# Kernel optimization log

Measured on AMD Instinct MI355X. Metric: run time of the kernel, lower is better.

Reference implementation:

```python
import jax, jax.numpy as jnp
import numpy as np

B, S, D, H, DK, DV = 2, 2048, 1024, 16, 64, 64


def setup_inputs() -> dict:
    key = jax.random.key(0)
    ks = jax.random.split(key, 12)
    s = 0.02
    return {
        "q": jax.random.normal(ks[0], (B, S, D), jnp.float32),
        "k": jax.random.normal(ks[1], (B, S, D), jnp.float32),
        "v": jax.random.normal(ks[2], (B, S, D), jnp.float32),
        "attn_mask": jax.random.bernoulli(ks[3], 0.1, (B, S, S)),
        "wq": jax.random.normal(ks[4], (D, H * DK), jnp.float32) * s,
        "bq": jnp.zeros((H * DK,), jnp.float32),
        "wk": jax.random.normal(ks[5], (D, H * DK), jnp.float32) * s,
        "bk": jnp.zeros((H * DK,), jnp.float32),
        "wv": jax.random.normal(ks[6], (D, H * DV), jnp.float32) * s,
        "bv": jnp.zeros((H * DV,), jnp.float32),
        "wo": jax.random.normal(ks[7], (H * DV, D), jnp.float32) * s,
        "bo": jnp.zeros((D,), jnp.float32),
        "gamma": jnp.ones((D,), jnp.float32),
        "beta": jnp.zeros((D,), jnp.float32),
    }


def reference(q, k, v, attn_mask, wq, bq, wk, bk, wv, bv, wo, bo, gamma, beta):
    residual = q
    # projections -> [B, H, S, dk/dv]
    qh = (q @ wq + bq).reshape(B, S, H, DK).transpose(0, 2, 1, 3)
    kh = (k @ wk + bk).reshape(B, S, H, DK).transpose(0, 2, 1, 3)
    vh = (v @ wv + bv).reshape(B, S, H, DV).transpose(0, 2, 1, 3)
    scores = jnp.einsum("bhqd,bhkd->bhqk", qh, kh) / np.sqrt(DK).astype(np.float32)
    scores = jnp.where(attn_mask[:, None, :, :], jnp.float32(-1e9), scores)
    attn = jax.nn.softmax(scores, axis=-1)
    context = jnp.einsum("bhqk,bhkd->bhqd", attn, vh)
    context = context.transpose(0, 2, 1, 3).reshape(B, S, H * DV)
    out = context @ wo + bo + residual
    # LayerNorm (eps=1e-5, torch default)
    mu = out.mean(-1, keepdims=True)
    var = out.var(-1, keepdims=True)
    out = (out - mu) * jax.lax.rsqrt(var + 1e-5) * gamma + beta
    return out, attn
```

## Files before the change

### kernel.cpp

```cpp
#include <hip/hip_runtime.h>
#include <hip/hip_bf16.h>

#define BB 2
#define SS 2048
#define DD 1024
#define HH 16
#define DKV 64

typedef __attribute__((ext_vector_type(8))) short short8;
typedef __attribute__((ext_vector_type(4))) short short4_t;
typedef __attribute__((ext_vector_type(4))) float f32x4;

#define MFMA16(a, b, c) __builtin_amdgcn_mfma_f32_16x16x32_bf16(a, b, c, 0, 0, 0)

__device__ __forceinline__ short f2bf(float f) {
    __hip_bfloat16 h = __float2bfloat16(f);
    union { __hip_bfloat16 h; short s; } u;
    u.h = h;
    return u.s;
}

__global__ __launch_bounds__(256) void proj3_kernel(
    const float* __restrict__ A0, const float* __restrict__ A1, const float* __restrict__ A2,
    const float* __restrict__ W0, const float* __restrict__ W1, const float* __restrict__ W2,
    const float* __restrict__ bq, const float* __restrict__ bk, const float* __restrict__ bv,
    __hip_bfloat16* __restrict__ o0, __hip_bfloat16* __restrict__ o1, __hip_bfloat16* __restrict__ o2,
    const int* __restrict__ mask, unsigned long long* __restrict__ bits)
{
    const int t = threadIdx.x;
    const int lane = t & 63;
    const int wave = t >> 6;

    if (blockIdx.z == 0) {
        const int bid = blockIdx.y * 32 + blockIdx.x;
        const int base = bid * 512 + wave * 128;
        #pragma unroll 4
        for (int wi = base; wi < base + 128; ++wi) {
            const int mv = mask[(size_t)wi * 64 + lane];
            const unsigned long long bal = __ballot(mv != 0);
            if (lane == 0) bits[wi] = bal;
        }
        return;
    }

    const int z = blockIdx.z - 1;
    const float* A = (z == 0) ? A0 : (z == 1) ? A1 : A2;
    const float* W = (z == 0) ? W0 : (z == 1) ? W1 : W2;
    const float* bias = (z == 0) ? bq : (z == 1) ? bk : bv;
    __hip_bfloat16* outh = (z == 0) ? o0 : (z == 1) ? o1 : o2;

    __shared__ __align__(16) short As[128][40];
    __shared__ __align__(16) short Bs[128][40];
    const int wm = wave >> 1, wn = wave & 1;
    const int m0 = blockIdx.x * 128, n0 = blockIdx.y * 128;
    const int lr = lane & 15;
    const int kb = (lane >> 4) * 8;

    f32x4 acc[4][4] = {};

    for (int k0 = 0; k0 < DD; k0 += 32) {
        __syncthreads();
        {
            const int row = t >> 1, kk = (t & 1) * 16;
            const float* src = A + (size_t)(m0 + row) * DD + k0 + kk;
            float4 fa = *(const float4*)(src);
            float4 fb = *(const float4*)(src + 4);
            float4 fc = *(const float4*)(src + 8);
            float4 fd = *(const float4*)(src + 12);
            short8 v0 = { f2bf(fa.x), f2bf(fa.y), f2bf(fa.z), f2bf(fa.w),
                          f2bf(fb.x), f2bf(fb.y), f2bf(fb.z), f2bf(fb.w) };
            short8 v1 = { f2bf(fc.x), f2bf(fc.y), f2bf(fc.z), f2bf(fc.w),
                          f2bf(fd.x), f2bf(fd.y), f2bf(fd.z), f2bf(fd.w) };
            *(short8*)&As[row][kk]     = v0;
            *(short8*)&As[row][kk + 8] = v1;
        }
        {
            const int kk = t >> 3, c0 = (t & 7) * 16;
            const float* src = W + (size_t)(k0 + kk) * DD + n0 + c0;
            #pragma unroll
            for (int i = 0; i < 16; i += 4) {
                float4 f = *(const float4*)(src + i);
                Bs[c0 + i + 0][kk] = f2bf(f.x);
                Bs[c0 + i + 1][kk] = f2bf(f.y);
                Bs[c0 + i + 2][kk] = f2bf(f.z);
                Bs[c0 + i + 3][kk] = f2bf(f.w);
            }
        }
        __syncthreads();
        short8 af[4], bfr[4];
        #pragma unroll
        for (int i = 0; i < 4; i++) af[i]  = *(const short8*)&As[wm * 64 + i * 16 + lr][kb];
        #pragma unroll
        for (int j = 0; j < 4; j++) bfr[j] = *(const short8*)&Bs[wn * 64 + j * 16 + lr][kb];
        #pragma unroll
        for (int i = 0; i < 4; i++)
            #pragma unroll
            for (int j = 0; j < 4; j++)
                acc[i][j] = MFMA16(af[i], bfr[j], acc[i][j]);
    }

    if (z != 2) {
        #pragma unroll
        for (int j = 0; j < 4; j++) {
            const int col = n0 + wn * 64 + j * 16 + lr;
            const float bvv = bias[col];
            const int h = col >> 6, d = col & 63;
            #pragma unroll
            for (int i = 0; i < 4; i++) {
                #pragma unroll
                for (int r = 0; r < 4; r++) {
                    const int m = m0 + wm * 64 + i * 16 + (lane >> 4) * 4 + r;
                    const int b = m >> 11, s = m & (SS - 1);
                    outh[(((size_t)(b * HH + h)) * SS + s) * DKV + d] =
                        __float2bfloat16(acc[i][j][r] + bvv);
                }
            }
        }
    } else {
        short* vT = (short*)outh;
        #pragma unroll
        for (int j = 0; j < 4; j++) {
            const int col = n0 + wn * 64 + j * 16 + lr;
            const float bvv = bias[col];
            const int h = col >> 6, d = col & 63;
            #pragma unroll
            for (int i = 0; i < 4; i++) {
                const int m = m0 + wm * 64 + i * 16 + (lane >> 4) * 4;
                const int b = m >> 11, s = m & (SS - 1);
                short4_t pk;
                #pragma unroll
                for (int r = 0; r < 4; r++) pk[r] = f2bf(acc[i][j][r] + bvv);
                *(short4_t*)(vT + ((size_t)(b * HH + h) * DKV + d) * SS + s) = pk;
            }
        }
    }
}

__global__ __launch_bounds__(256) void outproj_kernel(
    const __hip_bfloat16* __restrict__ Actx, const float* __restrict__ W,
    const float* __restrict__ bias, const float* __restrict__ resid,
    float* __restrict__ out)
{
    __shared__ __align__(16) short As[128][40];
    __shared__ __align__(16) short Bs[128][40];
    const int t = threadIdx.x;
    const int lane = t & 63;
    const int wave = t >> 6;
    const int wm = wave >> 1, wn = wave & 1;
    const int m0 = blockIdx.x * 128, n0 = blockIdx.y * 128;
    const int lr = lane & 15;
    const int kb = (lane >> 4) * 8;

    f32x4 acc[4][4] = {};

    for (int k0 = 0; k0 < DD; k0 += 32) {
        __syncthreads();
        {
            const int row = t >> 1, kk = (t & 1) * 16;
            const short8* src = (const short8*)((const short*)Actx + (size_t)(m0 + row) * DD + k0 + kk);
            *(short8*)&As[row][kk]     = src[0];
            *(short8*)&As[row][kk + 8] = src[1];
        }
        {
            const int kk = t >> 3, c0 = (t & 7) * 16;
            const float* src = W + (size_t)(k0 + kk) * DD + n0 + c0;
            #pragma unroll
            for (int i = 0; i < 16; i += 4) {
                float4 f = *(const float4*)(src + i);
                Bs[c0 + i + 0][kk] = f2bf(f.x);
                Bs[c0 + i + 1][kk] = f2bf(f.y);
                Bs[c0 + i + 2][kk] = f2bf(f.z);
                Bs[c0 + i + 3][kk] = f2bf(f.w);
            }
        }
        __syncthreads();
        short8 af[4], bfr[4];
        #pragma unroll
        for (int i = 0; i < 4; i++) af[i]  = *(const short8*)&As[wm * 64 + i * 16 + lr][kb];
        #pragma unroll
        for (int j = 0; j < 4; j++) bfr[j] = *(const short8*)&Bs[wn * 64 + j * 16 + lr][kb];
        #pragma unroll
        for (int i = 0; i < 4; i++)
            #pragma unroll
            for (int j = 0; j < 4; j++)
                acc[i][j] = MFMA16(af[i], bfr[j], acc[i][j]);
    }

    #pragma unroll
    for (int j = 0; j < 4; j++) {
        const int col = n0 + wn * 64 + j * 16 + lr;
        const float bvv = bias[col];
        #pragma unroll
        for (int i = 0; i < 4; i++) {
            #pragma unroll
            for (int r = 0; r < 4; r++) {
                const int m = m0 + wm * 64 + i * 16 + (lane >> 4) * 4 + r;
                out[(size_t)m * DD + col] = acc[i][j][r] + bvv + resid[(size_t)m * DD + col];
            }
        }
    }
}

__global__ __launch_bounds__(512) void attn_compute_kernel(
    const __hip_bfloat16* __restrict__ qh, const __hip_bfloat16* __restrict__ kh,
    const __hip_bfloat16* __restrict__ vT, const unsigned long long* __restrict__ bits,
    float* __restrict__ linvb, __hip_bfloat16* __restrict__ ctx)
{
    __shared__ __align__(16) short Ks[2][64][72];
    __shared__ __align__(16) short Vs[2][64][72];
    __shared__ __align__(16) short Ps[8][16][72];
    const int t = threadIdx.x, lane = t & 63, w = t >> 6;

    const int logical = (blockIdx.x & 7) * 64 + (blockIdx.x >> 3);
    const int qt = logical & 15;
    const int bh = logical >> 4;
    const int h = bh & (HH - 1);
    const int b = bh >> 4;
    const int q0w = qt * 128 + w * 16;
    const size_t headbase = (size_t)bh * SS * DKV;
    const int lr = lane & 15;
    const int kb = (lane >> 4) * 8;
    const int Q4 = lane >> 4;
    const int rbase = Q4 * 4;

    const short* kbase = (const short*)kh + headbase;
    const short* vbase = (const short*)vT + (size_t)bh * DKV * SS;
    const unsigned long long* bitrow = bits + ((size_t)b * SS + q0w) * (SS / 64);

    const int srow = t >> 3, sc8 = (t & 7) * 8;
    const short* kstg = kbase + (size_t)srow * DKV + sc8;
    const short* vstg = vbase + (size_t)srow * SS + sc8;

    const short* qrp = (const short*)qh + headbase + (size_t)(q0w + lr) * DKV;
    const short8 aq0 = *(const short8*)(qrp + kb);
    const short8 aq1 = *(const short8*)(qrp + 32 + kb);

    float lsum[4] = {0.f, 0.f, 0.f, 0.f};
    f32x4 cacc[4] = {};

    {
        short8 kreg = *(const short8*)(kstg);
        short8 vreg = *(const short8*)(vstg);
        *(short8*)&Ks[0][srow][sc8] = kreg;
        *(short8*)&Vs[0][srow][sc8] = vreg;
        __syncthreads();
        for (int kt = 0; kt < 32; ++kt) {
            const int cur = kt & 1;
            if (kt + 1 < 32) {
                kreg = *(const short8*)(kstg + (size_t)(kt + 1) * 64 * DKV);
                vreg = *(const short8*)(vstg + (size_t)(kt + 1) * 64);
            }
            f32x4 sc[4];
            #pragma unroll
            for (int fc = 0; fc < 4; ++fc) {
                short8 bk0 = *(const short8*)&Ks[cur][fc * 16 + lr][kb];
                short8 bk1 = *(const short8*)&Ks[cur][fc * 16 + lr][32 + kb];
                f32x4 s = {0.f, 0.f, 0.f, 0.f};
                s = MFMA16(aq0, bk0, s);
                s = MFMA16(aq1, bk1, s);
                sc[fc] = s;
            }
            unsigned long long mw[4];
            #pragma unroll
            for (int r = 0; r < 4; ++r)
                mw[r] = bitrow[(size_t)(rbase + r) * (SS / 64) + kt];
            #pragma unroll
            for (int fc = 0; fc < 4; ++fc)
                #pragma unroll
                for (int r = 0; r < 4; ++r) {
                    const bool masked = (mw[r] >> (fc * 16 + lr)) & 1ull;
                    const float p = masked ? 0.f : __expf(sc[fc][r] * 0.125f);
                    lsum[r] += p;
                    Ps[w][rbase + r][fc * 16 + lr] = f2bf(p);
                }
            short8 ap0 = *(const short8*)&Ps[w][lr][kb];
            short8 ap1 = *(const short8*)&Ps[w][lr][32 + kb];
            #pragma unroll
            for (int fd = 0; fd < 4; ++fd) {
                short8 bv0 = *(const short8*)&Vs[cur][fd * 16 + lr][kb];
                short8 bv1 = *(const short8*)&Vs[cur][fd * 16 + lr][32 + kb];
                cacc[fd] = MFMA16(ap0, bv0, cacc[fd]);
                cacc[fd] = MFMA16(ap1, bv1, cacc[fd]);
            }
            if (kt + 1 < 32) {
                *(short8*)&Ks[cur ^ 1][srow][sc8] = kreg;
                *(short8*)&Vs[cur ^ 1][srow][sc8] = vreg;
            }
            __syncthreads();
        }
    }
    #pragma unroll
    for (int r = 0; r < 4; r++) {
        float s = lsum[r];
        s += __shfl_xor(s, 1);
        s += __shfl_xor(s, 2);
        s += __shfl_xor(s, 4);
        s += __shfl_xor(s, 8);
        lsum[r] = s;
    }
    float linv[4];
    #pragma unroll
    for (int r = 0; r < 4; r++) linv[r] = 1.f / lsum[r];

    if (lr == 0) {
        #pragma unroll
        for (int r = 0; r < 4; r++)
            linvb[(size_t)bh * SS + q0w + rbase + r] = linv[r];
    }

    #pragma unroll
    for (int fd = 0; fd < 4; ++fd)
        #pragma unroll
        for (int r = 0; r < 4; r++) {
            const int qrow = q0w + rbase + r;
            ctx[((size_t)b * SS + qrow) * DD + h * DKV + fd * 16 + lr] =
                __float2bfloat16(cacc[fd][r] * linv[r]);
        }
}

__global__ __launch_bounds__(256) void attn_store_kernel(
    const __hip_bfloat16* __restrict__ qh, const __hip_bfloat16* __restrict__ kh,
    const unsigned long long* __restrict__ bits, const float* __restrict__ linvb,
    float* __restrict__ attn)
{
    __shared__ __align__(16) short Ks[512][72];
    const int t = threadIdx.x, lane = t & 63, w = t >> 6;
    const int qt = blockIdx.x;
    const int kc = blockIdx.y;
    const int bh = blockIdx.z;
    const int b = bh >> 4;
    const int q0w = qt * 64 + w * 16;
    const int k0c = kc * 512;
    const size_t headbase = (size_t)bh * SS * DKV;
    const int lr = lane & 15;
    const int kb = (lane >> 4) * 8;
    const int Q4 = lane >> 4;
    const int rbase = Q4 * 4;

    {
        const short* kbase = (const short*)kh + headbase + (size_t)k0c * DKV;
        const int c8 = (t & 7) * 8;
        #pragma unroll
        for (int sweep = 0; sweep < 16; ++sweep) {
            const int row = (t >> 3) + sweep * 32;
            *(short8*)&Ks[row][c8] = *(const short8*)(kbase + (size_t)row * DKV + c8);
        }
    }

    const short* qrp = (const short*)qh + headbase + (size_t)(q0w + lr) * DKV;
    const short8 aq0 = *(const short8*)(qrp + kb);
    const short8 aq1 = *(const short8*)(qrp + 32 + kb);

    float linv[4];
    #pragma unroll
    for (int r = 0; r < 4; ++r)
        linv[r] = linvb[(size_t)bh * SS + q0w + rbase + r];

    const unsigned long long* bitrow = bits + ((size_t)b * SS + q0w) * (SS / 64);
    float* arow = attn + ((size_t)bh * SS + q0w) * SS + k0c;

    __syncthreads();

    for (int g = 0; g < 8; ++g) {
        unsigned long long mw[4];
        #pragma unroll
        for (int r = 0; r < 4; ++r)
            mw[r] = bitrow[(size_t)(rbase + r) * (SS / 64) + kc * 8 + g];
        #pragma unroll
        for (int fc = 0; fc < 4; ++fc) {
            const int col = g * 64 + fc * 16;
            short8 bk0 = *(const short8*)&Ks[col + lr][kb];
            short8 bk1 = *(const short8*)&Ks[col + lr][32 + kb];
            f32x4 s = {0.f, 0.f, 0.f, 0.f};
            s = MFMA16(aq0, bk0, s);
            s = MFMA16(aq1, bk1, s);
            #pragma unroll
            for (int r = 0; r < 4; ++r) {
                const bool masked = (mw[r] >> (fc * 16 + lr)) & 1ull;
                const float p = masked ? 0.f : __expf(s[r] * 0.125f) * linv[r];
                arow[(size_t)(rbase + r) * SS + col + lr] = p;
            }
        }
    }
}

__global__ __launch_bounds__(256) void ln_kernel(
    float* __restrict__ io, const float* __restrict__ g, const float* __restrict__ bta)
{
    const int row = blockIdx.x;
    const int t = threadIdx.x;
    float* p = io + (size_t)row * DD;
    float4 x = *(float4*)(p + t * 4);
    float s  = x.x + x.y + x.z + x.w;
    float s2 = x.x * x.x + x.y * x.y + x.z * x.z + x.w * x.w;
    #pragma unroll
    for (int off = 32; off; off >>= 1) {
        s  += __shfl_xor(s, off);
        s2 += __shfl_xor(s2, off);
    }
    __shared__ float as_[4], bs_[4];
    const int w = t >> 6, l = t & 63;
    if (!l) { as_[w] = s; bs_[w] = s2; }
    __syncthreads();
    s  = as_[0] + as_[1] + as_[2] + as_[3];
    s2 = bs_[0] + bs_[1] + bs_[2] + bs_[3];
    const float mu  = s * (1.f / DD);
    const float var = s2 * (1.f / DD) - mu * mu;
    const float rs  = rsqrtf(var + 1e-5f);
    float4 gv = *(const float4*)(g + t * 4);
    float4 bv = *(const float4*)(bta + t * 4);
    float4 o;
    o.x = (x.x - mu) * rs * gv.x + bv.x;
    o.y = (x.y - mu) * rs * gv.y + bv.y;
    o.z = (x.z - mu) * rs * gv.z + bv.z;
    o.w = (x.w - mu) * rs * gv.w + bv.w;
    *(float4*)(p + t * 4) = o;
}

extern "C" void kernel_launch(void* const* d_in, const int* in_sizes, int n_in,
                              void* d_out, int out_size, void* d_ws, size_t ws_size,
                              hipStream_t stream)
{
    (void)in_sizes; (void)n_in; (void)out_size; (void)ws_size;
    const float* q     = (const float*)d_in[0];
    const float* k     = (const float*)d_in[1];
    const float* v     = (const float*)d_in[2];
    const int*   mask  = (const int*)d_in[3];
    const float* wq    = (const float*)d_in[4];
    const float* bq    = (const float*)d_in[5];
    const float* wk    = (const float*)d_in[6];
    const float* bk    = (const float*)d_in[7];
    const float* wv    = (const float*)d_in[8];
    const float* bv    = (const float*)d_in[9];
    const float* wo    = (const float*)d_in[10];
    const float* bo    = (const float*)d_in[11];
    const float* gamma = (const float*)d_in[12];
    const float* beta  = (const float*)d_in[13];

    float* out  = (float*)d_out;
    float* attn = out + (size_t)BB * SS * DD;

    const size_t hsz = (size_t)BB * HH * SS * DKV;
    __hip_bfloat16* qhp = (__hip_bfloat16*)d_ws;
    __hip_bfloat16* khp = qhp + hsz;
    __hip_bfloat16* vTp = khp + hsz;
    __hip_bfloat16* ctx = vTp + hsz;
    unsigned long long* bits = (unsigned long long*)(ctx + hsz);
    float* linvb = (float*)(bits + (size_t)BB * SS * (SS / 64));

    dim3 gg(32, 8, 4);
    proj3_kernel<<<gg, 256, 0, stream>>>(q, k, v, wq, wk, wv, bq, bk, bv,
                                         qhp, khp, vTp, mask, bits);
    attn_compute_kernel<<<BB * HH * 16, 512, 0, stream>>>(qhp, khp, vTp, bits, linvb, ctx);
    dim3 gs(32, 4, BB * HH);
    attn_store_kernel<<<gs, 256, 0, stream>>>(qhp, khp, bits, linvb, attn);
    dim3 go(32, 8);
    outproj_kernel<<<go, 256, 0, stream>>>(ctx, wo, bo, q, out);
    ln_kernel<<<BB * SS, 256, 0, stream>>>(out, gamma, beta);
}
```

Before: 393.2 us.

## Pre-transpose weights to bf16 once per call and raise MFMA wave priority

```diff
diff --git a/kernel.cpp b/kernel.cpp
--- a/kernel.cpp
+++ b/kernel.cpp
@@ -20,9 +20,37 @@
     return u.s;
 }
 
+__global__ __launch_bounds__(256) void wtrans_kernel(
+    const float* __restrict__ w0, const float* __restrict__ w1,
+    const float* __restrict__ w2, const float* __restrict__ w3,
+    short* __restrict__ o0, short* __restrict__ o1,
+    short* __restrict__ o2, short* __restrict__ o3)
+{
+    const int z = blockIdx.z;
+    const float* W = (z == 0) ? w0 : (z == 1) ? w1 : (z == 2) ? w2 : w3;
+    short* O = (z == 0) ? o0 : (z == 1) ? o1 : (z == 2) ? o2 : o3;
+    __shared__ short T[64][72];
+    const int t = threadIdx.x;
+    const int k0 = blockIdx.x * 64, n0 = blockIdx.y * 64;
+    const int row = t >> 2, c = (t & 3) * 16;
+    const float* src = W + (size_t)(k0 + row) * DD + n0 + c;
+    #pragma unroll
+    for (int i = 0; i < 16; i += 4) {
+        float4 f = *(const float4*)(src + i);
+        T[c + i + 0][row] = f2bf(f.x);
+        T[c + i + 1][row] = f2bf(f.y);
+        T[c + i + 2][row] = f2bf(f.z);
+        T[c + i + 3][row] = f2bf(f.w);
+    }
+    __syncthreads();
+    const int nr = t >> 2, kc = (t & 3) * 16;
+    *(short8*)(O + (size_t)(n0 + nr) * DD + k0 + kc)     = *(const short8*)&T[nr][kc];
+    *(short8*)(O + (size_t)(n0 + nr) * DD + k0 + kc + 8) = *(const short8*)&T[nr][kc + 8];
+}
+
 __global__ __launch_bounds__(256) void proj3_kernel(
     const float* __restrict__ A0, const float* __restrict__ A1, const float* __restrict__ A2,
-    const float* __restrict__ W0, const float* __restrict__ W1, const float* __restrict__ W2,
+    const short* __restrict__ WT0, const short* __restrict__ WT1, const short* __restrict__ WT2,
     const float* __restrict__ bq, const float* __restrict__ bk, const float* __restrict__ bv,
     __hip_bfloat16* __restrict__ o0, __hip_bfloat16* __restrict__ o1, __hip_bfloat16* __restrict__ o2,
     const int* __restrict__ mask, unsigned long long* __restrict__ bits)
@@ -44,8 +72,8 @@
     }
 
     const int z = blockIdx.z - 1;
-    const float* A = (z == 0) ? A0 : (z == 1) ? A1 : A2;
-    const float* W = (z == 0) ? W0 : (z == 1) ? W1 : W2;
+    const float* A  = (z == 0) ? A0 : (z == 1) ? A1 : A2;
+    const short* WT = (z == 0) ? WT0 : (z == 1) ? WT1 : WT2;
     const float* bias = (z == 0) ? bq : (z == 1) ? bk : bv;
     __hip_bfloat16* outh = (z == 0) ? o0 : (z == 1) ? o1 : o2;
 
@@ -55,14 +83,14 @@
     const int m0 = blockIdx.x * 128, n0 = blockIdx.y * 128;
     const int lr = lane & 15;
     const int kb = (lane >> 4) * 8;
+    const int row2 = t >> 1, kk2 = (t & 1) * 16;
 
     f32x4 acc[4][4] = {};
 
     for (int k0 = 0; k0 < DD; k0 += 32) {
         __syncthreads();
         {
-            const int row = t >> 1, kk = (t & 1) * 16;
-            const float* src = A + (size_t)(m0 + row) * DD + k0 + kk;
+            const float* src = A + (size_t)(m0 + row2) * DD + k0 + kk2;
             float4 fa = *(const float4*)(src);
             float4 fb = *(const float4*)(src + 4);
             float4 fc = *(const float4*)(src + 8);
@@ -71,20 +99,13 @@
                           f2bf(fb.x), f2bf(fb.y), f2bf(fb.z), f2bf(fb.w) };
             short8 v1 = { f2bf(fc.x), f2bf(fc.y), f2bf(fc.z), f2bf(fc.w),
                           f2bf(fd.x), f2bf(fd.y), f2bf(fd.z), f2bf(fd.w) };
-            *(short8*)&As[row][kk]     = v0;
-            *(short8*)&As[row][kk + 8] = v1;
+            *(short8*)&As[row2][kk2]     = v0;
+            *(short8*)&As[row2][kk2 + 8] = v1;
         }
         {
-            const int kk = t >> 3, c0 = (t & 7) * 16;
-            const float* src = W + (size_t)(k0 + kk) * DD + n0 + c0;
-            #pragma unroll
-            for (int i = 0; i < 16; i += 4) {
-                float4 f = *(const float4*)(src + i);
-                Bs[c0 + i + 0][kk] = f2bf(f.x);
-                Bs[c0 + i + 1][kk] = f2bf(f.y);
-                Bs[c0 + i + 2][kk] = f2bf(f.z);
-                Bs[c0 + i + 3][kk] = f2bf(f.w);
-            }
+            const short8* srcw = (const short8*)(WT + (size_t)(n0 + row2) * DD + k0 + kk2);
+            *(short8*)&Bs[row2][kk2]     = srcw[0];
+            *(short8*)&Bs[row2][kk2 + 8] = srcw[1];
         }
         __syncthreads();
         short8 af[4], bfr[4];
@@ -137,7 +158,7 @@
 }
 
 __global__ __launch_bounds__(256) void outproj_kernel(
-    const __hip_bfloat16* __restrict__ Actx, const float* __restrict__ W,
+    const __hip_bfloat16* __restrict__ Actx, const short* __restrict__ WT,
     const float* __restrict__ bias, const float* __restrict__ resid,
     float* __restrict__ out)
 {
@@ -150,28 +171,21 @@
     const int m0 = blockIdx.x * 128, n0 = blockIdx.y * 128;
     const int lr = lane & 15;
     const int kb = (lane >> 4) * 8;
+    const int row2 = t >> 1, kk2 = (t & 1) * 16;
 
     f32x4 acc[4][4] = {};
 
     for (int k0 = 0; k0 < DD; k0 += 32) {
         __syncthreads();
         {
-            const int row = t >> 1, kk = (t & 1) * 16;
-            const short8* src = (const short8*)((const short*)Actx + (size_t)(m0 + row) * DD + k0 + kk);
-            *(short8*)&As[row][kk]     = src[0];
-            *(short8*)&As[row][kk + 8] = src[1];
+            const short8* src = (const short8*)((const short*)Actx + (size_t)(m0 + row2) * DD + k0 + kk2);
+            *(short8*)&As[row2][kk2]     = src[0];
+            *(short8*)&As[row2][kk2 + 8] = src[1];
         }
         {
-            const int kk = t >> 3, c0 = (t & 7) * 16;
-            const float* src = W + (size_t)(k0 + kk) * DD + n0 + c0;
-            #pragma unroll
-            for (int i = 0; i < 16; i += 4) {
-                float4 f = *(const float4*)(src + i);
-                Bs[c0 + i + 0][kk] = f2bf(f.x);
-                Bs[c0 + i + 1][kk] = f2bf(f.y);
-                Bs[c0 + i + 2][kk] = f2bf(f.z);
-                Bs[c0 + i + 3][kk] = f2bf(f.w);
-            }
+            const short8* srcw = (const short8*)(WT + (size_t)(n0 + row2) * DD + k0 + kk2);
+            *(short8*)&Bs[row2][kk2]     = srcw[0];
+            *(short8*)&Bs[row2][kk2 + 8] = srcw[1];
         }
         __syncthreads();
         short8 af[4], bfr[4];
@@ -251,6 +265,7 @@
                 vreg = *(const short8*)(vstg + (size_t)(kt + 1) * 64);
             }
             f32x4 sc[4];
+            __builtin_amdgcn_s_setprio(1);
             #pragma unroll
             for (int fc = 0; fc < 4; ++fc) {
                 short8 bk0 = *(const short8*)&Ks[cur][fc * 16 + lr][kb];
@@ -260,6 +275,7 @@
                 s = MFMA16(aq1, bk1, s);
                 sc[fc] = s;
             }
+            __builtin_amdgcn_s_setprio(0);
             unsigned long long mw[4];
             #pragma unroll
             for (int r = 0; r < 4; ++r)
@@ -275,6 +291,7 @@
                 }
             short8 ap0 = *(const short8*)&Ps[w][lr][kb];
             short8 ap1 = *(const short8*)&Ps[w][lr][32 + kb];
+            __builtin_amdgcn_s_setprio(1);
             #pragma unroll
             for (int fd = 0; fd < 4; ++fd) {
                 short8 bv0 = *(const short8*)&Vs[cur][fd * 16 + lr][kb];
@@ -282,6 +299,7 @@
                 cacc[fd] = MFMA16(ap0, bv0, cacc[fd]);
                 cacc[fd] = MFMA16(ap1, bv1, cacc[fd]);
             }
+            __builtin_amdgcn_s_setprio(0);
             if (kt + 1 < 32) {
                 *(short8*)&Ks[cur ^ 1][srow][sc8] = kreg;
                 *(short8*)&Vs[cur ^ 1][srow][sc8] = vreg;
@@ -447,14 +465,21 @@
     __hip_bfloat16* ctx = vTp + hsz;
     unsigned long long* bits = (unsigned long long*)(ctx + hsz);
     float* linvb = (float*)(bits + (size_t)BB * SS * (SS / 64));
+    short* wtq = (short*)(linvb + (size_t)BB * HH * SS);
+    short* wtk = wtq + (size_t)DD * DD;
+    short* wtv = wtk + (size_t)DD * DD;
+    short* wto = wtv + (size_t)DD * DD;
+
+    dim3 gw(16, 16, 4);
+    wtrans_kernel<<<gw, 256, 0, stream>>>(wq, wk, wv, wo, wtq, wtk, wtv, wto);
 
     dim3 gg(32, 8, 4);
-    proj3_kernel<<<gg, 256, 0, stream>>>(q, k, v, wq, wk, wv, bq, bk, bv,
+    proj3_kernel<<<gg, 256, 0, stream>>>(q, k, v, wtq, wtk, wtv, bq, bk, bv,
                                          qhp, khp, vTp, mask, bits);
     attn_compute_kernel<<<BB * HH * 16, 512, 0, stream>>>(qhp, khp, vTp, bits, linvb, ctx);
     dim3 gs(32, 4, BB * HH);
     attn_store_kernel<<<gs, 256, 0, stream>>>(qhp, khp, bits, linvb, attn);
     dim3 go(32, 8);
-    outproj_kernel<<<go, 256, 0, stream>>>(ctx, wo, bo, q, out);
+    outproj_kernel<<<go, 256, 0, stream>>>(ctx, wto, bo, q, out);
     ln_kernel<<<BB * SS, 256, 0, stream>>>(out, gamma, beta);
 }
```

Measured after the change: 369.8 us. -5.9%, faster.
